# Kernel tuning notes

Measured on AMD Instinct MI355X. Metric: run time of the kernel, lower is better.

## Reference

```python
import jax, jax.numpy as jnp
import numpy as np

B, DYN, STAT, HALF, U, NOBS = 65536, 128, 64, 64, 16, 20
H1, H2, NEULER = 512, 512, 4
ZIN = DYN + STAT  # 192, H_net input dim


def setup_inputs() -> dict:
    key = jax.random.key(0)
    ks = jax.random.split(key, 13)
    def lin(kw, fan_in, shape):
        return jax.random.normal(kw, shape, dtype=jnp.float32) * (1.0 / np.sqrt(fan_in))
    return {
        "z_dyn": jax.random.normal(ks[0], (B, DYN), dtype=jnp.float32),
        "z_static": jax.random.normal(ks[1], (B, STAT), dtype=jnp.float32),
        "dt": jnp.float32(1.0),
        "ut": jax.random.normal(ks[2], (B, U), dtype=jnp.float32),
        "W1": lin(ks[3], ZIN, (H1, ZIN)), "b1": jnp.zeros((H1,), jnp.float32),
        "W2": lin(ks[4], H1, (H2, H1)), "b2": jnp.zeros((H2,), jnp.float32),
        "W3": lin(ks[5], H2, (1, H2)), "b3": jnp.zeros((1,), jnp.float32),
        "B_ctrl": jax.random.normal(ks[6], (HALF, U), dtype=jnp.float32) * (1.0 / np.sqrt(U)),
        "C": jax.random.normal(ks[7], (NOBS, DYN), dtype=jnp.float32) * (1.0 / np.sqrt(DYN)),
        "D": jax.random.normal(ks[8], (NOBS, U), dtype=jnp.float32) * (1.0 / np.sqrt(U)),
    }


def _H(zf, W1, b1, W2, b2, W3, b3):
    # [B, ZIN] -> scalar-per-row energy [B, 1]
    h = jax.nn.softplus(zf @ W1.T + b1)
    h = jax.nn.softplus(h @ W2.T + b2)
    return h @ W3.T + b3


def reference(z_dyn, z_static, dt, ut, W1, b1, W2, b2, W3, b3, B_ctrl, C, D):
    h = dt / NEULER
    grad_H = jax.grad(lambda zf: _H(zf, W1, b1, W2, b2, W3, b3).sum())
    z = z_dyn
    for _ in range(NEULER):  # fixed small Euler loop
        # torch detaches z before autograd.grad -> stop_gradient here
        zf = jax.lax.stop_gradient(jnp.concatenate([z, z_static], axis=-1))
        dH = grad_H(zf)            # [B, ZIN]
        dHdq = dH[:, :HALF]
        dHdp = dH[:, HALF:DYN]
        rhs = jnp.concatenate([dHdp, -dHdq + ut @ B_ctrl.T], axis=-1)
        z = z + h * rhs
    yt = z @ C.T + (ut * dt) @ D.T
    return z, yt
```

## Files before the change

kernel.cpp:

```cpp
#include <hip/hip_runtime.h>
#include <hip/hip_bf16.h>
#include <math.h>

typedef __bf16 bf16_t;
typedef __bf16 bf16x8 __attribute__((ext_vector_type(8)));
typedef __bf16 bf16x4 __attribute__((ext_vector_type(4)));
typedef float floatx4 __attribute__((ext_vector_type(4)));

#define BATCH 65536L
#define ROWS 64
#define MFMA __builtin_amdgcn_mfma_f32_16x16x32_bf16


__device__ __forceinline__ float softplus_f(float x) {
  const float l = __logf(1.f + __expf(x));
  return (x > 15.f) ? x : l;
}
__device__ __forceinline__ float sigmoid_f(float x) {
  return __builtin_amdgcn_rcpf(1.f + __expf(-x));
}

__device__ __forceinline__ void store_frag(char* buf, int NKT, int mf, int c0, int lr, bf16x4 v) {
  const int kt = c0 >> 5, lkp = (c0 & 31) >> 3, j0 = c0 & 7;
  *(bf16x4*)(buf + (((mf * NKT + kt) * 64) + lr + 16 * lkp) * 16 + j0 * 2) = v;
}
__device__ __forceinline__ bf16x4 load_frag(const char* buf, int NKT, int mf, int c0, int lr) {
  const int kt = c0 >> 5, lkp = (c0 & 31) >> 3, j0 = c0 & 7;
  return *(const bf16x4*)(buf + (((mf * NKT + kt) * 64) + lr + 16 * lkp) * 16 + j0 * 2);
}


template<int MF, int KT, int NT, int NF>
__device__ __forceinline__ void gemmP(const char* Abuf, const bf16_t* W, int ntb,
                                      int lane, floatx4 (&acc)[MF][NF])
{
  const char* wp = (const char*)W + (ntb * 64 + lane) * 16;
  const char* ap = Abuf + lane * 16;
  bf16x8 bv0[NF], bv1[NF];
  bf16x8 aA[MF], aB[MF];
#pragma unroll
  for (int nf = 0; nf < NF; ++nf) bv0[nf] = *(const bf16x8*)(wp + nf * 1024);
#pragma unroll
  for (int m = 0; m < MF; ++m) aA[m] = *(const bf16x8*)(ap + m * KT * 1024);
#pragma unroll 1
  for (int kt = 0; kt < KT; kt += 2) {
#pragma unroll
    for (int nf = 0; nf < NF; ++nf)
      bv1[nf] = *(const bf16x8*)(wp + NT * 1024 + nf * 1024);
#pragma unroll
    for (int m = 0; m < MF; ++m)
      aB[m] = *(const bf16x8*)(ap + 1024 + m * KT * 1024);
    __builtin_amdgcn_s_setprio(1);
#pragma unroll
    for (int m = 0; m < MF; ++m)
#pragma unroll
      for (int nf = 0; nf < NF; ++nf)
        acc[m][nf] = MFMA(bv0[nf], aA[m], acc[m][nf], 0, 0, 0);
    __builtin_amdgcn_s_setprio(0);
    if (kt + 2 < KT) {
#pragma unroll
      for (int nf = 0; nf < NF; ++nf)
        bv0[nf] = *(const bf16x8*)(wp + 2 * NT * 1024 + nf * 1024);
#pragma unroll
      for (int m = 0; m < MF; ++m)
        aA[m] = *(const bf16x8*)(ap + 2048 + m * KT * 1024);
    }
    __builtin_amdgcn_s_setprio(1);
#pragma unroll
    for (int m = 0; m < MF; ++m)
#pragma unroll
      for (int nf = 0; nf < NF; ++nf)
        acc[m][nf] = MFMA(bv1[nf], aB[m], acc[m][nf], 0, 0, 0);
    __builtin_amdgcn_s_setprio(0);
    wp += 2 * NT * 1024;
    ap += 2048;
  }
}

__device__ __forceinline__ void gemm_g1(const char* zf, const char* zs, const bf16_t* W,
                                        int ntb, int lane, floatx4 (&acc)[4][2])
{
  const char* wp = (const char*)W + (ntb * 64 + lane) * 16;
  bf16x8 bv0[2], bv1[2];
#pragma unroll
  for (int nf = 0; nf < 2; ++nf) bv0[nf] = *(const bf16x8*)(wp + nf * 1024);
#pragma unroll 1
  for (int kt = 0; kt < 6; kt += 2) {
    const char* ab = (kt < 4) ? (zf + kt * 1024 + lane * 16)
                              : (zs + (kt - 4) * 1024 + lane * 16);
    const int  ms = (kt < 4) ? 4096 : 2048;
#pragma unroll
    for (int nf = 0; nf < 2; ++nf)
      bv1[nf] = *(const bf16x8*)(wp + 32 * 1024 + nf * 1024);
    bf16x8 a[4];
#pragma unroll
    for (int m = 0; m < 4; ++m) a[m] = *(const bf16x8*)(ab + m * ms);
    __builtin_amdgcn_s_setprio(1);
#pragma unroll
    for (int m = 0; m < 4; ++m)
#pragma unroll
      for (int nf = 0; nf < 2; ++nf)
        acc[m][nf] = MFMA(bv0[nf], a[m], acc[m][nf], 0, 0, 0);
    __builtin_amdgcn_s_setprio(0);
    if (kt + 2 < 6) {
#pragma unroll
      for (int nf = 0; nf < 2; ++nf)
        bv0[nf] = *(const bf16x8*)(wp + 64 * 1024 + nf * 1024);
    }
#pragma unroll
    for (int m = 0; m < 4; ++m) a[m] = *(const bf16x8*)(ab + 1024 + m * ms);
    __builtin_amdgcn_s_setprio(1);
#pragma unroll
    for (int m = 0; m < 4; ++m)
#pragma unroll
      for (int nf = 0; nf < 2; ++nf)
        acc[m][nf] = MFMA(bv1[nf], a[m], acc[m][nf], 0, 0, 0);
    __builtin_amdgcn_s_setprio(0);
    wp += 64 * 1024;
  }
}


__global__ __launch_bounds__(512, 1)
void ham_fused(const float* __restrict__ z_dyn, const float* __restrict__ z_static,
               const float* __restrict__ dtp, const float* __restrict__ ut,
               const float* __restrict__ b1, const float* __restrict__ b2,
               const bf16_t* __restrict__ W1s, const bf16_t* __restrict__ W2s,
               const bf16_t* __restrict__ W2ts, const bf16_t* __restrict__ W1ts,
               const float* __restrict__ Bc, const float* __restrict__ Cm,
               const float* __restrict__ Dm,
               float* __restrict__ z_out, float* __restrict__ yt_out)
{
  __shared__ __align__(16) char bufX[65536];
  __shared__ __align__(16) char bufY[65536];
  __shared__ __align__(16) char zst[8192];
  __shared__ __align__(16) float uBs[64 * 68];

  const int tid  = threadIdx.x;
  const int lane = tid & 63;
  const int w    = tid >> 6;
  const int lr   = lane & 15;
  const int lk   = lane >> 4;
  const long rb  = (long)blockIdx.x * ROWS;

  const float dtv = __builtin_bit_cast(float,
      __builtin_amdgcn_readfirstlane(__builtin_bit_cast(int, dtp[0])));
  const float hstep = dtv * 0.25f;
  const int   pcb   = ((w + 4) & 7) * 16;

  for (int e = tid; e < 64 * 16; e += 512) ((float*)bufX)[e] = Bc[e];
  for (int e = tid; e < ROWS * 64; e += 512) {
    const int rr = e >> 6, cc = e & 63;
    const float v = __builtin_nontemporal_load(z_static + (rb + rr) * 64 + cc);
    const int kt = cc >> 5, lkp = (cc & 31) >> 3, j = cc & 7;
    *(bf16_t*)(zst + ((((rr >> 4) * 2 + kt) * 64) + (rr & 15) + 16 * lkp) * 16 + j * 2) = (bf16_t)v;
  }
  floatx4 zp[4];
#pragma unroll
  for (int m = 0; m < 4; ++m)
    zp[m] = __builtin_nontemporal_load(
        (const floatx4*)(z_dyn + (rb + m * 16 + lr) * 128 + pcb + lk * 4));
  __syncthreads();

  for (int e = tid; e < ROWS * 64; e += 512) {
    const int rr = e >> 6, cc = e & 63;
    const float* ur = ut + (rb + rr) * 16;
    const float* bc = (const float*)bufX + cc * 16;
    float s = 0.f;
#pragma unroll
    for (int u = 0; u < 16; ++u) s += ur[u] * bc[u];
    uBs[rr * 68 + cc] = s;
  }

  for (int s = 0; s < 4; ++s) {
#pragma unroll
    for (int m = 0; m < 4; ++m) {
      bf16x4 o;
#pragma unroll
      for (int i = 0; i < 4; ++i) o[i] = (bf16_t)zp[m][i];
      store_frag(bufY, 4, m, pcb + lk * 4, lr, o);
    }
    __syncthreads();

#pragma unroll 1
    for (int p = 0; p < 2; ++p) {
      floatx4 acc[4][2] = {};
      gemm_g1(bufY, zst, W1s, p * 16 + w * 2, lane, acc);
#pragma unroll
      for (int m = 0; m < 4; ++m)
#pragma unroll
        for (int nf = 0; nf < 2; ++nf) {
          const int c0 = p * 256 + w * 32 + nf * 16 + lk * 4;
          const floatx4 b4 = *(const floatx4*)(b1 + c0);
          bf16x4 h4;
#pragma unroll
          for (int i = 0; i < 4; ++i) h4[i] = (bf16_t)softplus_f(acc[m][nf][i] + b4[i]);
          store_frag(bufX, 16, m, c0, lr, h4);
        }
    }
    __syncthreads();

#pragma unroll 1
    for (int p = 0; p < 2; ++p) {
      floatx4 acc[4][2] = {};
      gemmP<4, 16, 32, 2>(bufX, W2s, p * 16 + w * 2, lane, acc);
#pragma unroll
      for (int m = 0; m < 4; ++m)
#pragma unroll
        for (int nf = 0; nf < 2; ++nf) {
          const int c0 = p * 256 + w * 32 + nf * 16 + lk * 4;
          const floatx4 b4 = *(const floatx4*)(b2 + c0);
          bf16x4 g4;
#pragma unroll
          for (int i = 0; i < 4; ++i) g4[i] = (bf16_t)sigmoid_f(acc[m][nf][i] + b4[i]);
          store_frag(bufY, 16, m, c0, lr, g4);
        }
    }
    __syncthreads();

#pragma unroll 1
    for (int p = 0; p < 2; ++p) {
      floatx4 acc[4][2] = {};
      gemmP<4, 16, 32, 2>(bufY, W2ts, p * 16 + w * 2, lane, acc);
#pragma unroll
      for (int m = 0; m < 4; ++m)
#pragma unroll
        for (int nf = 0; nf < 2; ++nf) {
          const int c0 = p * 256 + w * 32 + nf * 16 + lk * 4;
          const bf16x4 h4 = load_frag(bufX, 16, m, c0, lr);
          bf16x4 g4;
#pragma unroll
          for (int i = 0; i < 4; ++i) {
            const float s1 = 1.f - __expf(-(float)h4[i]);
            g4[i] = (bf16_t)(s1 * acc[m][nf][i]);
          }
          store_frag(bufX, 16, m, c0, lr, g4);
        }
    }
    __syncthreads();

    {
      floatx4 a4[4][1] = {};
      gemmP<4, 16, 8, 1>(bufX, W1ts, w, lane, a4);
#pragma unroll
      for (int m = 0; m < 4; ++m) {
        if (w < 4) {
          const float* ub = &uBs[(m * 16 + lr) * 68 + w * 16 + lk * 4];
#pragma unroll
          for (int i = 0; i < 4; ++i) zp[m][i] += hstep * (ub[i] - a4[m][0][i]);
        } else {
#pragma unroll
          for (int i = 0; i < 4; ++i) zp[m][i] += hstep * a4[m][0][i];
        }
      }
    }
  }

#pragma unroll
  for (int m = 0; m < 4; ++m)
    __builtin_nontemporal_store(zp[m],
        (floatx4*)(z_out + (rb + m * 16 + lr) * 128 + pcb + lk * 4));
  __syncthreads();
#pragma unroll
  for (int m = 0; m < 4; ++m)
    *(floatx4*)((float*)bufX + (m * 16 + lr) * 132 + pcb + lk * 4) = zp[m];
  for (int e = tid; e < 20 * 128; e += 512) {
    const int o = e >> 7, i = e & 127;
    ((float*)bufY)[o * 132 + i] = Cm[e];
  }
  for (int e = tid; e < 20 * 16; e += 512) ((float*)zst)[e] = Dm[e];
  __syncthreads();

  for (int q = tid; q < ROWS * 20; q += 512) {
    const int rr = q / 20, o = q - rr * 20;
    const float* zr = (const float*)bufX + rr * 132;
    const float* cr = (const float*)bufY + o * 132;
    float sm = 0.f;
#pragma unroll 4
    for (int i = 0; i < 128; ++i) sm += zr[i] * cr[i];
    float su = 0.f;
#pragma unroll
    for (int u = 0; u < 16; ++u)
      su += __builtin_nontemporal_load(ut + (rb + rr) * 16 + u) * ((const float*)zst)[o * 16 + u];
    __builtin_nontemporal_store(sm + dtv * su, yt_out + (rb + rr) * 20 + o);
  }
}


__global__ void prep_shuffle(const float* W1, const float* W2, const float* W3,
                             bf16_t* W1s, bf16_t* W2s, bf16_t* W2ts, bf16_t* W1ts)
{
  const long idx = (long)blockIdx.x * 256 + threadIdx.x;
  const long S1 = 98304, S2 = 262144, S3 = 262144, S4 = 65536;
  if (idx < S1) {
    const long e = idx;
    const int j = (int)(e & 7), ln = (int)((e >> 3) & 63), tile = (int)(e >> 9);
    const int nt = tile & 31, kt = tile >> 5;
    const int srow = nt * 16 + (ln & 15), scol = kt * 32 + (ln >> 4) * 8 + j;
    W1s[e] = (bf16_t)W1[srow * 192 + scol];
  } else if (idx < S1 + S2) {
    const long e = idx - S1;
    const int j = (int)(e & 7), ln = (int)((e >> 3) & 63), tile = (int)(e >> 9);
    const int nt = tile & 31, kt = tile >> 5;
    const int srow = nt * 16 + (ln & 15), scol = kt * 32 + (ln >> 4) * 8 + j;
    W2s[e] = (bf16_t)W2[srow * 512 + scol];
  } else if (idx < S1 + S2 + S3) {
    const long e = idx - S1 - S2;
    const int j = (int)(e & 7), ln = (int)((e >> 3) & 63), tile = (int)(e >> 9);
    const int nt = tile & 31, kt = tile >> 5;
    const int srow = nt * 16 + (ln & 15), scol = kt * 32 + (ln >> 4) * 8 + j;
    W2ts[e] = (bf16_t)(W2[scol * 512 + srow] * W3[scol]);
  } else if (idx < S1 + S2 + S3 + S4) {
    const long e = idx - S1 - S2 - S3;
    const int j = (int)(e & 7), ln = (int)((e >> 3) & 63), tile = (int)(e >> 9);
    const int nt = tile & 7, kt = tile >> 3;
    const int srow = nt * 16 + (ln & 15), scol = kt * 32 + (ln >> 4) * 8 + j;
    W1ts[e] = (bf16_t)W1[scol * 192 + srow];
  }
}


extern "C" void kernel_launch(void* const* d_in, const int* in_sizes, int n_in,
                              void* d_out, int out_size, void* d_ws, size_t ws_size,
                              hipStream_t stream)
{
  const float* z_dyn    = (const float*)d_in[0];
  const float* z_static = (const float*)d_in[1];
  const float* dtp      = (const float*)d_in[2];
  const float* ut       = (const float*)d_in[3];
  const float* W1       = (const float*)d_in[4];
  const float* b1       = (const float*)d_in[5];
  const float* W2       = (const float*)d_in[6];
  const float* b2       = (const float*)d_in[7];
  const float* W3       = (const float*)d_in[8];
  const float* Bc       = (const float*)d_in[10];
  const float* Cm       = (const float*)d_in[11];
  const float* Dm       = (const float*)d_in[12];

  float* z_out  = (float*)d_out;
  float* yt_out = z_out + BATCH * 128;

  char* ws = (char*)d_ws;
  size_t off = 0;
  auto alloc = [&](size_t bytes) {
    char* p = ws + off;
    off = (off + bytes + 255) & ~(size_t)255;
    return p;
  };
  bf16_t* W1s  = (bf16_t*)alloc(98304 * 2);
  bf16_t* W2s  = (bf16_t*)alloc(262144 * 2);
  bf16_t* W2ts = (bf16_t*)alloc(262144 * 2);
  bf16_t* W1ts = (bf16_t*)alloc(65536 * 2);
  (void)ws_size; (void)in_sizes; (void)n_in; (void)out_size;

  prep_shuffle<<<2688, 256, 0, stream>>>(W1, W2, W3, W1s, W2s, W2ts, W1ts);
  ham_fused<<<(int)(BATCH / ROWS), 512, 0, stream>>>(
      z_dyn, z_static, dtp, ut, b1, b2, W1s, W2s, W2ts, W1ts, Bc, Cm, Dm, z_out, yt_out);
}
```

Before: 450.3 us.

## Double block to 1024 threads, splitting N-tiles across 16 waves and K in final GEMM

The fused kernel now launches 1024 threads (16 waves) per 64-row block instead of 512. Each wave owns one N-slice in the W1, W2 and W2^T GEMMs, replacing the two-pass loop over p. The last W1^T GEMM is split along K across the two wave halves, with partial sums reduced through shared memory behind an extra barrier. The aim is more waves in flight for latency hiding. The costs are a tighter register budget under launch_bounds(1024,4), an added sync and half the waves idling in the z update.

```diff
diff --git a/kernel.cpp b/kernel.cpp
--- a/kernel.cpp
+++ b/kernel.cpp
@@ -30,7 +30,7 @@
 }
 
 
-template<int MF, int KT, int NT, int NF>
+template<int MF, int KTL, int KS, int NT, int NF>
 __device__ __forceinline__ void gemmP(const char* Abuf, const bf16_t* W, int ntb,
                                       int lane, floatx4 (&acc)[MF][NF])
 {
@@ -41,15 +41,15 @@
 #pragma unroll
   for (int nf = 0; nf < NF; ++nf) bv0[nf] = *(const bf16x8*)(wp + nf * 1024);
 #pragma unroll
-  for (int m = 0; m < MF; ++m) aA[m] = *(const bf16x8*)(ap + m * KT * 1024);
+  for (int m = 0; m < MF; ++m) aA[m] = *(const bf16x8*)(ap + m * KTL * 1024);
 #pragma unroll 1
-  for (int kt = 0; kt < KT; kt += 2) {
+  for (int kt = 0; kt < KS; kt += 2) {
 #pragma unroll
     for (int nf = 0; nf < NF; ++nf)
       bv1[nf] = *(const bf16x8*)(wp + NT * 1024 + nf * 1024);
 #pragma unroll
     for (int m = 0; m < MF; ++m)
-      aB[m] = *(const bf16x8*)(ap + 1024 + m * KT * 1024);
+      aB[m] = *(const bf16x8*)(ap + 1024 + m * KTL * 1024);
     __builtin_amdgcn_s_setprio(1);
 #pragma unroll
     for (int m = 0; m < MF; ++m)
@@ -57,13 +57,13 @@
       for (int nf = 0; nf < NF; ++nf)
         acc[m][nf] = MFMA(bv0[nf], aA[m], acc[m][nf], 0, 0, 0);
     __builtin_amdgcn_s_setprio(0);
-    if (kt + 2 < KT) {
+    if (kt + 2 < KS) {
 #pragma unroll
       for (int nf = 0; nf < NF; ++nf)
         bv0[nf] = *(const bf16x8*)(wp + 2 * NT * 1024 + nf * 1024);
 #pragma unroll
       for (int m = 0; m < MF; ++m)
-        aA[m] = *(const bf16x8*)(ap + 2048 + m * KT * 1024);
+        aA[m] = *(const bf16x8*)(ap + 2048 + m * KTL * 1024);
     }
     __builtin_amdgcn_s_setprio(1);
 #pragma unroll
@@ -121,7 +121,7 @@
 }
 
 
-__global__ __launch_bounds__(512, 1)
+__global__ __launch_bounds__(1024, 4)
 void ham_fused(const float* __restrict__ z_dyn, const float* __restrict__ z_static,
                const float* __restrict__ dtp, const float* __restrict__ ut,
                const float* __restrict__ b1, const float* __restrict__ b2,
@@ -148,21 +148,23 @@
   const float hstep = dtv * 0.25f;
   const int   pcb   = ((w + 4) & 7) * 16;
 
-  for (int e = tid; e < 64 * 16; e += 512) ((float*)bufX)[e] = Bc[e];
-  for (int e = tid; e < ROWS * 64; e += 512) {
+  for (int e = tid; e < 64 * 16; e += 1024) ((float*)bufX)[e] = Bc[e];
+  for (int e = tid; e < ROWS * 64; e += 1024) {
     const int rr = e >> 6, cc = e & 63;
     const float v = __builtin_nontemporal_load(z_static + (rb + rr) * 64 + cc);
     const int kt = cc >> 5, lkp = (cc & 31) >> 3, j = cc & 7;
     *(bf16_t*)(zst + ((((rr >> 4) * 2 + kt) * 64) + (rr & 15) + 16 * lkp) * 16 + j * 2) = (bf16_t)v;
   }
   floatx4 zp[4];
-#pragma unroll
-  for (int m = 0; m < 4; ++m)
-    zp[m] = __builtin_nontemporal_load(
-        (const floatx4*)(z_dyn + (rb + m * 16 + lr) * 128 + pcb + lk * 4));
+  if (w < 8) {
+#pragma unroll
+    for (int m = 0; m < 4; ++m)
+      zp[m] = __builtin_nontemporal_load(
+          (const floatx4*)(z_dyn + (rb + m * 16 + lr) * 128 + pcb + lk * 4));
+  }
   __syncthreads();
 
-  for (int e = tid; e < ROWS * 64; e += 512) {
+  for (int e = tid; e < ROWS * 64; e += 1024) {
     const int rr = e >> 6, cc = e & 63;
     const float* ur = ut + (rb + rr) * 16;
     const float* bc = (const float*)bufX + cc * 16;
@@ -173,24 +175,25 @@
   }
 
   for (int s = 0; s < 4; ++s) {
-#pragma unroll
-    for (int m = 0; m < 4; ++m) {
-      bf16x4 o;
-#pragma unroll
-      for (int i = 0; i < 4; ++i) o[i] = (bf16_t)zp[m][i];
-      store_frag(bufY, 4, m, pcb + lk * 4, lr, o);
+    if (w < 8) {
+#pragma unroll
+      for (int m = 0; m < 4; ++m) {
+        bf16x4 o;
+#pragma unroll
+        for (int i = 0; i < 4; ++i) o[i] = (bf16_t)zp[m][i];
+        store_frag(bufY, 4, m, pcb + lk * 4, lr, o);
+      }
     }
     __syncthreads();
 
-#pragma unroll 1
-    for (int p = 0; p < 2; ++p) {
+    {
       floatx4 acc[4][2] = {};
-      gemm_g1(bufY, zst, W1s, p * 16 + w * 2, lane, acc);
+      gemm_g1(bufY, zst, W1s, w * 2, lane, acc);
 #pragma unroll
       for (int m = 0; m < 4; ++m)
 #pragma unroll
         for (int nf = 0; nf < 2; ++nf) {
-          const int c0 = p * 256 + w * 32 + nf * 16 + lk * 4;
+          const int c0 = w * 32 + nf * 16 + lk * 4;
           const floatx4 b4 = *(const floatx4*)(b1 + c0);
           bf16x4 h4;
 #pragma unroll
@@ -200,15 +203,14 @@
     }
     __syncthreads();
 
-#pragma unroll 1
-    for (int p = 0; p < 2; ++p) {
+    {
       floatx4 acc[4][2] = {};
-      gemmP<4, 16, 32, 2>(bufX, W2s, p * 16 + w * 2, lane, acc);
+      gemmP<4, 16, 16, 32, 2>(bufX, W2s, w * 2, lane, acc);
 #pragma unroll
       for (int m = 0; m < 4; ++m)
 #pragma unroll
         for (int nf = 0; nf < 2; ++nf) {
-          const int c0 = p * 256 + w * 32 + nf * 16 + lk * 4;
+          const int c0 = w * 32 + nf * 16 + lk * 4;
           const floatx4 b4 = *(const floatx4*)(b2 + c0);
           bf16x4 g4;
 #pragma unroll
@@ -218,15 +220,14 @@
     }
     __syncthreads();
 
-#pragma unroll 1
-    for (int p = 0; p < 2; ++p) {
+    {
       floatx4 acc[4][2] = {};
-      gemmP<4, 16, 32, 2>(bufY, W2ts, p * 16 + w * 2, lane, acc);
+      gemmP<4, 16, 16, 32, 2>(bufY, W2ts, w * 2, lane, acc);
 #pragma unroll
       for (int m = 0; m < 4; ++m)
 #pragma unroll
         for (int nf = 0; nf < 2; ++nf) {
-          const int c0 = p * 256 + w * 32 + nf * 16 + lk * 4;
+          const int c0 = w * 32 + nf * 16 + lk * 4;
           const bf16x4 h4 = load_frag(bufX, 16, m, c0, lr);
           bf16x4 g4;
 #pragma unroll
@@ -241,37 +242,52 @@
 
     {
       floatx4 a4[4][1] = {};
-      gemmP<4, 16, 8, 1>(bufX, W1ts, w, lane, a4);
-#pragma unroll
-      for (int m = 0; m < 4; ++m) {
-        if (w < 4) {
-          const float* ub = &uBs[(m * 16 + lr) * 68 + w * 16 + lk * 4];
-#pragma unroll
-          for (int i = 0; i < 4; ++i) zp[m][i] += hstep * (ub[i] - a4[m][0][i]);
-        } else {
-#pragma unroll
-          for (int i = 0; i < 4; ++i) zp[m][i] += hstep * a4[m][0][i];
+      const int nt4 = w & 7, kh = w >> 3;
+      gemmP<4, 16, 8, 8, 1>(bufX + kh * 8192, W1ts + kh * 32768, nt4, lane, a4);
+      float* pb = (float*)(bufY + 16384);
+      if (kh) {
+#pragma unroll
+        for (int m = 0; m < 4; ++m)
+          *(floatx4*)(pb + (m * 16 + lr) * 132 + nt4 * 16 + lk * 4) = a4[m][0];
+      }
+      __syncthreads();
+      if (!kh) {
+#pragma unroll
+        for (int m = 0; m < 4; ++m) {
+          const floatx4 pp = *(const floatx4*)(pb + (m * 16 + lr) * 132 + nt4 * 16 + lk * 4);
+          if (w < 4) {
+            const float* ub = &uBs[(m * 16 + lr) * 68 + w * 16 + lk * 4];
+#pragma unroll
+            for (int i = 0; i < 4; ++i) zp[m][i] += hstep * (ub[i] - (a4[m][0][i] + pp[i]));
+          } else {
+#pragma unroll
+            for (int i = 0; i < 4; ++i) zp[m][i] += hstep * (a4[m][0][i] + pp[i]);
+          }
         }
       }
     }
   }
 
-#pragma unroll
-  for (int m = 0; m < 4; ++m)
-    __builtin_nontemporal_store(zp[m],
-        (floatx4*)(z_out + (rb + m * 16 + lr) * 128 + pcb + lk * 4));
+  if (w < 8) {
+#pragma unroll
+    for (int m = 0; m < 4; ++m)
+      __builtin_nontemporal_store(zp[m],
+          (floatx4*)(z_out + (rb + m * 16 + lr) * 128 + pcb + lk * 4));
+  }
   __syncthreads();
-#pragma unroll
-  for (int m = 0; m < 4; ++m)
-    *(floatx4*)((float*)bufX + (m * 16 + lr) * 132 + pcb + lk * 4) = zp[m];
-  for (int e = tid; e < 20 * 128; e += 512) {
+  if (w < 8) {
+#pragma unroll
+    for (int m = 0; m < 4; ++m)
+      *(floatx4*)((float*)bufX + (m * 16 + lr) * 132 + pcb + lk * 4) = zp[m];
+  }
+  for (int e = tid; e < 20 * 128; e += 1024) {
     const int o = e >> 7, i = e & 127;
     ((float*)bufY)[o * 132 + i] = Cm[e];
   }
-  for (int e = tid; e < 20 * 16; e += 512) ((float*)zst)[e] = Dm[e];
+  for (int e = tid; e < 20 * 16; e += 1024) ((float*)zst)[e] = Dm[e];
   __syncthreads();
 
-  for (int q = tid; q < ROWS * 20; q += 512) {
+  for (int q = tid; q < ROWS * 20; q += 1024) {
     const int rr = q / 20, o = q - rr * 20;
     const float* zr = (const float*)bufX + rr * 132;
     const float* cr = (const float*)bufY + o * 132;
@@ -354,6 +370,6 @@
   (void)ws_size; (void)in_sizes; (void)n_in; (void)out_size;
 
   prep_shuffle<<<2688, 256, 0, stream>>>(W1, W2, W3, W1s, W2s, W2ts, W1ts);
-  ham_fused<<<(int)(BATCH / ROWS), 512, 0, stream>>>(
+  ham_fused<<<(int)(BATCH / ROWS), 1024, 0, stream>>>(
       z_dyn, z_static, dtp, ut, b1, b2, W1s, W2s, W2ts, W1ts, Bc, Cm, Dm, z_out, yt_out);
 }
```

Result: slower. 622.8 us (+38.3%).
